# Optimization experiments

Hardware: AMD Instinct MI355X
Metric: run time of the kernel (lower is better)

Reference implementation:

```python
import jax, jax.numpy as jnp
import numpy as np

B, S, D = 2, 2048, 1024
H, HK, HD = 16, 4, 64          # query heads, kv heads, head dim = D//H
WIN = 1024                     # sliding attention window
E, K, DH = 8, 2, 2048          # experts, top_k, expert hidden (== d_head ctor arg)
ATTN_EPS, FFN_EPS = 1e-5, 1e-6
ROPE_THETA = 10000.0


def setup_inputs() -> dict:
    key = jax.random.key(0)
    ks = jax.random.split(key, 9)
    sc = 0.02
    # real rotary frequencies for positions [start_pos, start_pos+S)
    start_pos = 0
    inv_freq = 1.0 / (ROPE_THETA ** (jnp.arange(0, HD, 2, dtype=jnp.float32) / HD))  # [HD//2]
    pos = jnp.arange(start_pos, start_pos + S, dtype=jnp.float32)
    ang = pos[:, None] * inv_freq[None, :]  # [S, HD//2]
    return {
        'x': jax.random.normal(ks[0], (B, S, D), jnp.float32),
        'freqs_cos': jnp.cos(ang),
        'freqs_sin': jnp.sin(ang),
        'attn_norm_w': jnp.ones((D,), jnp.float32),
        'wq': jax.random.normal(ks[1], (D, H * HD), jnp.float32) * sc,
        'wk': jax.random.normal(ks[2], (D, HK * HD), jnp.float32) * sc,
        'wv': jax.random.normal(ks[3], (D, HK * HD), jnp.float32) * sc,
        'wo': jax.random.normal(ks[4], (H * HD, D), jnp.float32) * sc,
        'ffn_norm_w': jnp.ones((D,), jnp.float32),
        'router_w': jax.random.normal(ks[5], (D, E), jnp.float32) * sc,
        'w1': jax.random.normal(ks[6], (E, D, DH), jnp.float32) * sc,
        'w2': jax.random.normal(ks[7], (E, DH, D), jnp.float32) * sc,
        'start_pos': start_pos,
    }


def _rmsnorm(x, w, eps):
    return x * jax.lax.rsqrt(jnp.mean(x * x, axis=-1, keepdims=True) + eps) * w


def _rope(t, cos, sin):
    # t: [B,S,N,HD]; cos/sin: [S,HD//2] -> complex rotation on consecutive pairs
    shp = t.shape
    t = t.reshape(shp[:-1] + (HD // 2, 2))
    t0, t1 = t[..., 0], t[..., 1]
    c = cos[None, :, None, :]
    s = sin[None, :, None, :]
    r = jnp.stack([t0 * c - t1 * s, t0 * s + t1 * c], axis=-1)
    return r.reshape(shp)


def reference(x, freqs_cos, freqs_sin, attn_norm_w, wq, wk, wv, wo,
              ffn_norm_w, router_w, w1, w2, start_pos):
    # ---- attention sublayer (RMSNorm -> GQA sliding-window attn) ----
    hn = _rmsnorm(x, attn_norm_w, ATTN_EPS)
    q = (hn @ wq).reshape(B, S, H, HD)
    k = (hn @ wk).reshape(B, S, HK, HD)
    v = (hn @ wv).reshape(B, S, HK, HD)
    q = _rope(q, freqs_cos, freqs_sin)
    k = _rope(k, freqs_cos, freqs_sin)
    rep = H // HK
    k = jnp.repeat(k, rep, axis=2)  # [B,S,H,HD]
    v = jnp.repeat(v, rep, axis=2)
    scale = 1.0 / np.sqrt(HD).astype(np.float32)
    scores = jnp.einsum('bqhd,bkhd->bhqk', q, k) * scale  # [B,H,S,S]
    qi = jnp.arange(S) + start_pos
    kj = jnp.arange(S) + start_pos
    mask = (kj[None, :] <= qi[:, None]) & (qi[:, None] - kj[None, :] < WIN)
    scores = jnp.where(mask[None, None], scores, jnp.float32(-1e30))
    attn = jax.nn.softmax(scores, axis=-1)
    o = jnp.einsum('bhqk,bkhd->bqhd', attn, v).reshape(B, S, H * HD)
    h = x + o @ wo

    # ---- MoE sublayer (RMSNorm -> router top-k -> expert FFNs) ----
    fn = _rmsnorm(h, ffn_norm_w, FFN_EPS).reshape(-1, D)  # [T,D], T=B*S
    probs = jax.nn.softmax(fn @ router_w, axis=-1)        # [T,E]
    top_vals, top_idx = jax.lax.top_k(probs, K)           # [T,K]
    gates = top_vals / jnp.sum(top_vals, axis=-1, keepdims=True)
    gmat = jnp.sum(jax.nn.one_hot(top_idx, E, dtype=fn.dtype) * gates[..., None], axis=1)  # [T,E]
    moe = jnp.zeros_like(fn)
    for e in range(E):  # fixed small expert count
        moe = moe + gmat[:, e:e + 1] * (jax.nn.silu(fn @ w1[e]) @ w2[e])
    return h + moe.reshape(B, S, D)
```

## Files before the change

kernel.cpp:

```cpp
#include <hip/hip_runtime.h>
#include <hip/hip_bf16.h>

using bf16 = __hip_bfloat16;
typedef __attribute__((ext_vector_type(8))) short bf16x8;
typedef __attribute__((ext_vector_type(4))) short short4v;
typedef __attribute__((ext_vector_type(4))) float f32x4;

#define DEV static __device__ __forceinline__

DEV float b2f(bf16 v) { return __bfloat162float(v); }
DEV bf16  f2b(float f) { return __float2bfloat16(f); }
DEV short bbits(float f) { bf16 h = __float2bfloat16(f); short u; __builtin_memcpy(&u, &h, 2); return u; }
DEV float sb2f(short s) {
  unsigned u = ((unsigned)(unsigned short)s) << 16;
  float f; __builtin_memcpy(&f, &u, 4); return f;
}

#define GL2LDS(g, l)                                                        \
  __builtin_amdgcn_global_load_lds(                                         \
      (const __attribute__((address_space(1))) void*)(g),                   \
      (__attribute__((address_space(3))) void*)(l), 16, 0, 0)

__global__ __launch_bounds__(256) void transpose_convert(
    const float* __restrict__ src, bf16* __restrict__ dst, int K, int N) {
  __shared__ float tile[64][65];
  int n0 = blockIdx.x * 64, k0 = blockIdx.y * 64;
  src += (size_t)blockIdx.z * K * N;
  dst += (size_t)blockIdx.z * K * N;
  int t = threadIdx.x;
  int rr = t >> 4, cc = (t & 15) * 4;
#pragma unroll
  for (int p = 0; p < 4; ++p) {
    int r = rr + p * 16;
    const float4 v = *(const float4*)&src[(size_t)(k0 + r) * N + n0 + cc];
    tile[r][cc] = v.x; tile[r][cc + 1] = v.y; tile[r][cc + 2] = v.z; tile[r][cc + 3] = v.w;
  }
  __syncthreads();
#pragma unroll
  for (int p = 0; p < 4; ++p) {
    int nr = rr + p * 16;
    short4v o;
    o[0] = bbits(tile[cc + 0][nr]);
    o[1] = bbits(tile[cc + 1][nr]);
    o[2] = bbits(tile[cc + 2][nr]);
    o[3] = bbits(tile[cc + 3][nr]);
    *(short4v*)&dst[(size_t)(n0 + nr) * K + k0 + cc] = o;
  }
}

__global__ __launch_bounds__(256) void rmsnorm_kernel(
    const float* __restrict__ x, const float* __restrict__ w,
    bf16* __restrict__ o, float eps) {
  int row = blockIdx.x;
  const float* xr = x + (size_t)row * 1024;
  int t = threadIdx.x;
  float4 v = *(const float4*)&xr[t * 4];
  float ss = v.x * v.x + v.y * v.y + v.z * v.z + v.w * v.w;
#pragma unroll
  for (int d = 32; d; d >>= 1) ss += __shfl_down(ss, d);
  __shared__ float red[4];
  if ((t & 63) == 0) red[t >> 6] = ss;
  __syncthreads();
  float sum = red[0] + red[1] + red[2] + red[3];
  float sc = rsqrtf(sum * (1.f / 1024.f) + eps);
  const float4 wv = *(const float4*)&w[t * 4];
  short4v pk;
  pk[0] = bbits(v.x * sc * wv.x);
  pk[1] = bbits(v.y * sc * wv.y);
  pk[2] = bbits(v.z * sc * wv.z);
  pk[3] = bbits(v.w * sc * wv.w);
  *(short4v*)&o[(size_t)row * 1024 + t * 4] = pk;
}

__global__ __launch_bounds__(256) void rmsnorm_router(
    const float* __restrict__ h, const float* __restrict__ w,
    const float* __restrict__ rw, bf16* __restrict__ fn,
    float* __restrict__ gates, int* __restrict__ eidx) {
  int row = blockIdx.x;
  const float* hr = h + (size_t)row * 1024;
  int t = threadIdx.x;
  float4 v = *(const float4*)&hr[t * 4];
  float ss = v.x * v.x + v.y * v.y + v.z * v.z + v.w * v.w;
#pragma unroll
  for (int d = 32; d; d >>= 1) ss += __shfl_down(ss, d);
  __shared__ float red[4];
  __shared__ float red2[4][8];
  if ((t & 63) == 0) red[t >> 6] = ss;
  __syncthreads();
  float sum = red[0] + red[1] + red[2] + red[3];
  float sc = rsqrtf(sum * (1.f / 1024.f) + 1e-6f);
  const float4 wv = *(const float4*)&w[t * 4];
  float f0 = v.x * sc * wv.x, f1 = v.y * sc * wv.y;
  float f2 = v.z * sc * wv.z, f3 = v.w * sc * wv.w;
  short4v pk;
  pk[0] = bbits(f0); pk[1] = bbits(f1); pk[2] = bbits(f2); pk[3] = bbits(f3);
  *(short4v*)&fn[(size_t)row * 1024 + t * 4] = pk;
  const float* rr = rw + (size_t)t * 4 * 8;
  float lg[8];
#pragma unroll
  for (int e = 0; e < 8; ++e)
    lg[e] = f0 * rr[e] + f1 * rr[8 + e] + f2 * rr[16 + e] + f3 * rr[24 + e];
#pragma unroll
  for (int d = 32; d; d >>= 1)
#pragma unroll
    for (int e = 0; e < 8; ++e) lg[e] += __shfl_down(lg[e], d);
  if ((t & 63) == 0)
#pragma unroll
    for (int e = 0; e < 8; ++e) red2[t >> 6][e] = lg[e];
  __syncthreads();
  if (t == 0) {
    float L[8];
#pragma unroll
    for (int e = 0; e < 8; ++e)
      L[e] = red2[0][e] + red2[1][e] + red2[2][e] + red2[3][e];
    int e0 = 0; float v0 = L[0];
#pragma unroll
    for (int e = 1; e < 8; ++e) if (L[e] > v0) { v0 = L[e]; e0 = e; }
    int e1 = -1; float v1 = -1e30f;
#pragma unroll
    for (int e = 0; e < 8; ++e) if (e != e0 && L[e] > v1) { v1 = L[e]; e1 = e; }
    float r1 = expf(v1 - v0);
    float den = 1.f + r1;
    gates[row * 2] = 1.f / den;
    gates[row * 2 + 1] = r1 / den;
    eidx[row * 2] = e0;
    eidx[row * 2 + 1] = e1;
  }
}

template <int MODE>
__global__ __launch_bounds__(256) void gemm_bt(
    const bf16* __restrict__ A, const bf16* __restrict__ Bt,
    int M, int N, int Kd,
    bf16* __restrict__ outb, bf16* __restrict__ outk, bf16* __restrict__ outv,
    float* __restrict__ outf, const float* __restrict__ resid,
    const float* __restrict__ fcos, const float* __restrict__ fsin,
    const int* __restrict__ counts, const int* __restrict__ offsets,
    const int* __restrict__ tok, const float* __restrict__ gatel) {
  int count = M, off = 0;
  const bf16* Ap = A;
  const bf16* Bp = Bt;
  int mb, nb;
  if (MODE == 2 || MODE == 3) {
    int e = blockIdx.y;
    count = counts[e]; off = offsets[e];
    Bp = Bt + (size_t)e * Kd * N;
    if (MODE == 3) Ap = A + (size_t)off * Kd;
    mb = blockIdx.z * 128; nb = blockIdx.x * 128;
  } else {
    int gx = gridDim.x;
    int flat = blockIdx.y * gx + blockIdx.x;
    int cpx = (gx * gridDim.y) >> 3;
    int swz = (flat & 7) * cpx + (flat >> 3);
    mb = (swz / gx) * 128; nb = (swz % gx) * 128;
  }
  if (mb >= count) return;

  __shared__ __align__(16) bf16 As[2][128 * 32];
  __shared__ __align__(16) bf16 Bs[2][128 * 32];

  int t = threadIdx.x;
  int lane = t & 63, wid = t >> 6;

  const bf16* agl[2];
  const bf16* bgl[2];
#pragma unroll
  for (int iss = 0; iss < 2; ++iss) {
    int p = iss * 256 + wid * 64 + lane;
    int row = p >> 2, cs = p & 3;
    int c = cs ^ (row & 3);
    int m = mb + row;
    const bf16* abase;
    if (MODE == 2) {
      int tokid = (m < count) ? tok[off + m] : 0;
      abase = A + (size_t)tokid * Kd;
    } else {
      int mm = (m < count) ? m : 0;
      abase = Ap + (size_t)mm * Kd;
    }
    agl[iss] = abase + c * 8;
    bgl[iss] = Bp + (size_t)(nb + row) * Kd + c * 8;
  }

  int wr = (wid >> 1) * 64, wc = (wid & 1) * 64;
  int lr = lane & 15, lkc = lane >> 4;

  auto stage = [&](int buf, int kt) {
#pragma unroll
    for (int iss = 0; iss < 2; ++iss) {
      GL2LDS(agl[iss] + kt * 32, &As[buf][(iss * 256 + wid * 64) * 8]);
      GL2LDS(bgl[iss] + kt * 32, &Bs[buf][(iss * 256 + wid * 64) * 8]);
    }
  };

  const f32x4 fzero = {0.f, 0.f, 0.f, 0.f};
  f32x4 acc[4][4];
#pragma unroll
  for (int i = 0; i < 4; ++i)
#pragma unroll
    for (int j = 0; j < 4; ++j) acc[i][j] = fzero;

  int nk = Kd >> 5;
  stage(0, 0);
  __syncthreads();
  for (int kt = 0; kt < nk; ++kt) {
    int cur = kt & 1;
    if (kt + 1 < nk) stage(cur ^ 1, kt + 1);
    bf16x8 af[4], bfr[4];
#pragma unroll
    for (int i = 0; i < 4; ++i) {
      int r = wr + i * 16 + lr;
      af[i] = *(const bf16x8*)&As[cur][r * 32 + ((lkc ^ (r & 3)) * 8)];
    }
#pragma unroll
    for (int j = 0; j < 4; ++j) {
      int r = wc + j * 16 + lr;
      bfr[j] = *(const bf16x8*)&Bs[cur][r * 32 + ((lkc ^ (r & 3)) * 8)];
    }
#pragma unroll
    for (int i = 0; i < 4; ++i)
#pragma unroll
      for (int j = 0; j < 4; ++j)
        acc[i][j] = __builtin_amdgcn_mfma_f32_16x16x32_bf16(af[i], bfr[j], acc[i][j], 0, 0, 0);
    __syncthreads();
  }

  int rq = lane >> 4;
#pragma unroll
  for (int i = 0; i < 4; ++i) {
#pragma unroll
    for (int j = 0; j < 4; ++j) {
      if (MODE == 5) {
        int n = nb + wc + j * 16 + lr;
        if (n >= 1280) {
          int vcol = n - 1280;
          int kh = vcol >> 6, d = vcol & 63;
          int m0 = mb + wr + i * 16 + rq * 4;
          int bb = m0 >> 11, s = m0 & 2047;
          short4v pk;
#pragma unroll
          for (int r = 0; r < 4; ++r) pk[r] = bbits(acc[i][j][r]);
          *(short4v*)&outv[((size_t)((bb * 4 + kh) * 64 + d)) * 2048 + s] = pk;
        } else {
          int ii = (n & 63) >> 1;
          bool odd = n & 1;
#pragma unroll
          for (int r = 0; r < 4; ++r) {
            int m = mb + wr + i * 16 + rq * 4 + r;
            int s = m & 2047;
            float v = acc[i][j][r];
            float vp = __shfl_xor(v, 1);
            float c = fcos[s * 32 + ii], sn = fsin[s * 32 + ii];
            float o = odd ? (vp * sn + v * c) : (v * c - vp * sn);
            if (n < 1024) outb[(size_t)m * 1024 + n] = f2b(o);
            else          outk[(size_t)m * 256 + (n - 1024)] = f2b(o);
          }
        }
      } else {
#pragma unroll
        for (int r = 0; r < 4; ++r) {
          int m = mb + wr + i * 16 + rq * 4 + r;
          int n = nb + wc + j * 16 + lr;
          float v = acc[i][j][r];
          if (MODE == 1) {
            outf[(size_t)m * N + n] = resid[(size_t)m * N + n] + v;
          } else if (MODE == 2) {
            if (m < count) {
              float sg = 1.f / (1.f + expf(-v));
              outb[(size_t)(off + m) * N + n] = f2b(v * sg);
            }
          } else if (MODE == 3) {
            if (m < count) {
              int row = off + m;
              outb[(size_t)row * N + n] = f2b(gatel[row] * v);
            }
          }
        }
      }
    }
  }
}

__global__ __launch_bounds__(256) void attn_kernel(
    const bf16* __restrict__ q, const bf16* __restrict__ kb,
    const bf16* __restrict__ vt, bf16* __restrict__ o) {
  int qb = blockIdx.x, h = blockIdx.y, b = blockIdx.z;
  int kh = h >> 2;
  int t = threadIdx.x;
  int lane = t & 63, wid = t >> 6;
  int lr = lane & 15, lkc = lane >> 4;
  int q0 = qb * 64;
  int qrow = q0 + wid * 16;

  __shared__ __align__(16) bf16 Ks[64 * 64];
  __shared__ __align__(16) bf16 Vs[64 * 64];
  __shared__ __align__(16) bf16 Ps[4][16 * 72];

  bf16x8 aq[2];
#pragma unroll
  for (int kk = 0; kk < 2; ++kk)
    aq[kk] = *(const bf16x8*)&q[(size_t)(b * 2048 + qrow + lr) * 1024 + h * 64 + kk * 32 + lkc * 8];

  const f32x4 fzero = {0.f, 0.f, 0.f, 0.f};
  f32x4 oacc[4];
  float mrun[4], lrun[4];
#pragma unroll
  for (int r = 0; r < 4; ++r) { oacc[r] = fzero; mrun[r] = -1e30f; lrun[r] = 0.f; }

  int klo = q0 - 1023; if (klo < 0) klo = 0;
  int tlo = klo >> 6, thi = q0 >> 6;
  int skey = t >> 3;
  int sch = t & 7;

  for (int kt = tlo; kt <= thi; ++kt) {
    int kbase = kt * 64;
#pragma unroll
    for (int pp = 0; pp < 2; ++pp) {
      int key = skey + pp * 32;
      bf16x8 kv = *(const bf16x8*)&kb[(size_t)(b * 2048 + kbase + key) * 256 + kh * 64 + sch * 8];
      *(bf16x8*)&Ks[key * 64 + ((sch ^ (key & 7)) * 8)] = kv;
      bf16x8 vv = *(const bf16x8*)&vt[((size_t)((b * 4 + kh) * 64 + key)) * 2048 + kbase + sch * 8];
      *(bf16x8*)&Vs[key * 64 + ((sch ^ (key & 7)) * 8)] = vv;
    }
    __syncthreads();

    f32x4 sacc[4];
#pragma unroll
    for (int nt = 0; nt < 4; ++nt) sacc[nt] = fzero;
#pragma unroll
    for (int nt = 0; nt < 4; ++nt)
#pragma unroll
      for (int kk = 0; kk < 2; ++kk) {
        int r = nt * 16 + lr;
        bf16x8 bk = *(const bf16x8*)&Ks[r * 64 + (((kk * 4 + lkc) ^ (r & 7)) * 8)];
        sacc[nt] = __builtin_amdgcn_mfma_f32_16x16x32_bf16(aq[kk], bk, sacc[nt], 0, 0, 0);
      }

    float sval[4][4], mt[4];
    int qg = qrow + lkc * 4;
#pragma unroll
    for (int r = 0; r < 4; ++r) mt[r] = -1e30f;
#pragma unroll
    for (int nt = 0; nt < 4; ++nt) {
      int kkey = kbase + nt * 16 + lr;
#pragma unroll
      for (int r = 0; r < 4; ++r) {
        float s = sacc[nt][r] * 0.125f;
        int qq = qg + r;
        bool valid = (kkey <= qq) && (qq - kkey < 1024);
        s = valid ? s : -1e30f;
        sval[nt][r] = s;
        mt[r] = fmaxf(mt[r], s);
      }
    }
#pragma unroll
    for (int d = 1; d < 16; d <<= 1)
#pragma unroll
      for (int r = 0; r < 4; ++r) mt[r] = fmaxf(mt[r], __shfl_xor(mt[r], d));
    float alpha[4], rs[4];
#pragma unroll
    for (int r = 0; r < 4; ++r) {
      float mn = fmaxf(mrun[r], mt[r]);
      alpha[r] = __expf(mrun[r] - mn);
      mrun[r] = mn;
      rs[r] = 0.f;
    }
#pragma unroll
    for (int nt = 0; nt < 4; ++nt)
#pragma unroll
      for (int r = 0; r < 4; ++r) {
        float pv = __expf(sval[nt][r] - mrun[r]);
        sval[nt][r] = pv;
        rs[r] += pv;
      }
#pragma unroll
    for (int d = 1; d < 16; d <<= 1)
#pragma unroll
      for (int r = 0; r < 4; ++r) rs[r] += __shfl_xor(rs[r], d);
#pragma unroll
    for (int r = 0; r < 4; ++r) lrun[r] = lrun[r] * alpha[r] + rs[r];
#pragma unroll
    for (int dt = 0; dt < 4; ++dt) {
      f32x4 t4 = oacc[dt];
#pragma unroll
      for (int r = 0; r < 4; ++r) t4[r] *= alpha[r];
      oacc[dt] = t4;
    }

    bf16* pw = &Ps[wid][0];
#pragma unroll
    for (int nt = 0; nt < 4; ++nt)
#pragma unroll
      for (int r = 0; r < 4; ++r)
        pw[(lkc * 4 + r) * 72 + nt * 16 + lr] = f2b(sval[nt][r]);
    __syncthreads();

    bf16x8 pa[2];
#pragma unroll
    for (int kk2 = 0; kk2 < 2; ++kk2)
      pa[kk2] = *(const bf16x8*)&pw[lr * 72 + kk2 * 32 + lkc * 8];
#pragma unroll
    for (int dt = 0; dt < 4; ++dt)
#pragma unroll
      for (int kk2 = 0; kk2 < 2; ++kk2) {
        int rrow = dt * 16 + lr;
        bf16x8 bv = *(const bf16x8*)&Vs[rrow * 64 + (((kk2 * 4 + lkc) ^ (rrow & 7)) * 8)];
        oacc[dt] = __builtin_amdgcn_mfma_f32_16x16x32_bf16(pa[kk2], bv, oacc[dt], 0, 0, 0);
      }
    __syncthreads();
  }

#pragma unroll
  for (int dt = 0; dt < 4; ++dt)
#pragma unroll
    for (int r = 0; r < 4; ++r) {
      int qq = qrow + lkc * 4 + r;
      int dd = dt * 16 + lr;
      o[(size_t)(b * 2048 + qq) * 1024 + h * 64 + dd] = f2b(oacc[dt][r] / lrun[r]);
    }
}

__global__ __launch_bounds__(1024) void moe_setup(
    const int* __restrict__ eidx, const float* __restrict__ gates,
    int* __restrict__ counts, int* __restrict__ offsets,
    int* __restrict__ tok, float* __restrict__ gatel, int* __restrict__ inv) {
  __shared__ int hist[8];
  __shared__ int cur[8];
  int t = threadIdx.x;
  if (t < 8) hist[t] = 0;
  __syncthreads();
  int e[8];
#pragma unroll
  for (int c = 0; c < 8; ++c) {
    e[c] = eidx[c * 1024 + t];
    atomicAdd(&hist[e[c]], 1);
  }
  __syncthreads();
  if (t == 0) {
    int o = 0;
#pragma unroll
    for (int i = 0; i < 8; ++i) {
      offsets[i] = o; cur[i] = o;
      int cnt = hist[i]; counts[i] = cnt; o += cnt;
    }
  }
  __syncthreads();
#pragma unroll
  for (int c = 0; c < 8; ++c) {
    int i = c * 1024 + t;
    int pos = atomicAdd(&cur[e[c]], 1);
    tok[pos] = i >> 1;
    gatel[pos] = gates[i];
    inv[i] = pos;
  }
}

__global__ __launch_bounds__(256) void final_add(
    const float* __restrict__ h, const bf16* __restrict__ y2,
    const int* __restrict__ inv, float* __restrict__ out) {
  int tokid = blockIdx.x;
  int t = threadIdx.x;
  int i0 = inv[tokid * 2], i1 = inv[tokid * 2 + 1];
  size_t base = (size_t)tokid * 1024 + t * 4;
  float4 a = *(const float4*)&h[base];
  short4v p0 = *(const short4v*)&y2[(size_t)i0 * 1024 + t * 4];
  short4v p1 = *(const short4v*)&y2[(size_t)i1 * 1024 + t * 4];
  float4 o;
  o.x = a.x + sb2f(p0[0]) + sb2f(p1[0]);
  o.y = a.y + sb2f(p0[1]) + sb2f(p1[1]);
  o.z = a.z + sb2f(p0[2]) + sb2f(p1[2]);
  o.w = a.w + sb2f(p0[3]) + sb2f(p1[3]);
  *(float4*)&out[base] = o;
}

extern "C" void kernel_launch(void* const* d_in, const int* in_sizes, int n_in,
                              void* d_out, int out_size, void* d_ws, size_t ws_size,
                              hipStream_t stream) {
  const float* x    = (const float*)d_in[0];
  const float* fcos = (const float*)d_in[1];
  const float* fsin = (const float*)d_in[2];
  const float* attw = (const float*)d_in[3];
  const float* wq   = (const float*)d_in[4];
  const float* wk   = (const float*)d_in[5];
  const float* wv   = (const float*)d_in[6];
  const float* wo   = (const float*)d_in[7];
  const float* ffnw = (const float*)d_in[8];
  const float* rw   = (const float*)d_in[9];
  const float* w1   = (const float*)d_in[10];
  const float* w2   = (const float*)d_in[11];
  float* out = (float*)d_out;

  const int M = 4096;
  char* p = (char*)d_ws;
  auto alloc = [&](size_t b) { char* r = p; p += (b + 255) & ~(size_t)255; return r; };

  bf16* hn     = (bf16*)alloc((size_t)M * 1024 * 2);
  bf16* qb     = (bf16*)alloc((size_t)M * 1024 * 2);
  bf16* kbuf   = (bf16*)alloc((size_t)M * 256 * 2);
  bf16* vt     = (bf16*)alloc((size_t)M * 256 * 2);
  bf16* ob     = (bf16*)alloc((size_t)M * 1024 * 2);
  float* hbuf  = (float*)alloc((size_t)M * 1024 * 4);
  bf16* fn     = (bf16*)alloc((size_t)M * 1024 * 2);
  bf16* wqkvt  = (bf16*)alloc((size_t)1536 * 1024 * 2);
  bf16* wot    = (bf16*)alloc((size_t)1024 * 1024 * 2);
  bf16* w1t    = (bf16*)alloc((size_t)8 * 2048 * 1024 * 2);
  bf16* w2t    = (bf16*)alloc((size_t)8 * 1024 * 2048 * 2);
  bf16* act    = (bf16*)alloc((size_t)8192 * 2048 * 2);
  bf16* y2     = (bf16*)alloc((size_t)8192 * 1024 * 2);
  float* gates = (float*)alloc((size_t)M * 2 * 4);
  int* eidx    = (int*)alloc((size_t)M * 2 * 4);
  int* counts  = (int*)alloc(8 * 4);
  int* offsets = (int*)alloc(8 * 4);
  int* tok     = (int*)alloc(8192 * 4);
  int* inv     = (int*)alloc(8192 * 4);
  float* gatel = (float*)alloc(8192 * 4);

  transpose_convert<<<dim3(16, 16, 1), 256, 0, stream>>>(wq, wqkvt, 1024, 1024);
  transpose_convert<<<dim3(4, 16, 1), 256, 0, stream>>>(wk, wqkvt + (size_t)1024 * 1024, 1024, 256);
  transpose_convert<<<dim3(4, 16, 1), 256, 0, stream>>>(wv, wqkvt + (size_t)1280 * 1024, 1024, 256);
  transpose_convert<<<dim3(16, 16, 1), 256, 0, stream>>>(wo, wot, 1024, 1024);
  transpose_convert<<<dim3(32, 16, 8), 256, 0, stream>>>(w1, w1t, 1024, 2048);
  transpose_convert<<<dim3(16, 32, 8), 256, 0, stream>>>(w2, w2t, 2048, 1024);

  rmsnorm_kernel<<<M, 256, 0, stream>>>(x, attw, hn, 1e-5f);

  gemm_bt<5><<<dim3(12, 32, 1), 256, 0, stream>>>(hn, wqkvt, M, 1536, 1024,
      qb, kbuf, vt, nullptr, nullptr, fcos, fsin, nullptr, nullptr, nullptr, nullptr);

  attn_kernel<<<dim3(32, 16, 2), 256, 0, stream>>>(qb, kbuf, vt, ob);

  gemm_bt<1><<<dim3(8, 32, 1), 256, 0, stream>>>(ob, wot, M, 1024, 1024,
      nullptr, nullptr, nullptr, hbuf, x, nullptr, nullptr, nullptr, nullptr, nullptr, nullptr);

  rmsnorm_router<<<M, 256, 0, stream>>>(hbuf, ffnw, rw, fn, gates, eidx);
  moe_setup<<<1, 1024, 0, stream>>>(eidx, gates, counts, offsets, tok, gatel, inv);

  gemm_bt<2><<<dim3(16, 8, 64), 256, 0, stream>>>(fn, w1t, M, 2048, 1024,
      act, nullptr, nullptr, nullptr, nullptr, nullptr, nullptr, counts, offsets, tok, nullptr);
  gemm_bt<3><<<dim3(8, 8, 64), 256, 0, stream>>>(act, w2t, M, 1024, 2048,
      y2, nullptr, nullptr, nullptr, nullptr, nullptr, nullptr, counts, offsets, tok, gatel);

  final_add<<<M, 256, 0, stream>>>(hbuf, y2, inv, out);
}
```

Measured before the change: 354.1 us.

## Add dedicated 256x128-tile MoE up-projection GEMM with 512 threads and 3-stage B pipeline

Replaces the generic gemm_bt<2> expert up-projection with a specialized kernel that uses 256-row M tiles, 8 waves per block, and a triple-buffered B / double-buffered A LDS pipeline with explicit vmcnt waits and raised MFMA priority. The larger M tile halves the number of times each expert weight tile is streamed and reduces the block count, and the deeper pipeline is meant to hide global-to-LDS latency. It trades higher LDS and register use (launch_bounds 512,1) and more wasted rows for experts whose token count is not a multiple of 256. Padding rows now clamp to the last valid token instead of token 0.

```diff
diff --git a/kernel.cpp b/kernel.cpp
--- a/kernel.cpp
+++ b/kernel.cpp
@@ -125,6 +125,120 @@
     gates[row * 2 + 1] = r1 / den;
     eidx[row * 2] = e0;
     eidx[row * 2 + 1] = e1;
+  }
+}
+
+__global__ __launch_bounds__(512, 1) void gemm_moe1(
+    const bf16* __restrict__ A, const bf16* __restrict__ Bt,
+    bf16* __restrict__ outb,
+    const int* __restrict__ counts, const int* __restrict__ offsets,
+    const int* __restrict__ tok) {
+  constexpr int Kd = 1024;
+  constexpr int NN = 2048;
+  constexpr int nk = Kd / 32;
+  int e = blockIdx.y;
+  int count = counts[e], off = offsets[e];
+  int mb = blockIdx.z * 256, nb = blockIdx.x * 128;
+  if (mb >= count) return;
+  const bf16* Bp = Bt + (size_t)e * Kd * NN;
+
+  __shared__ __align__(16) bf16 As[2][256 * 32];
+  __shared__ __align__(16) bf16 Bs[3][128 * 32];
+
+  int t = threadIdx.x;
+  int lane = t & 63, wid = t >> 6;
+  int wm = wid >> 1, wn = wid & 1;
+  int lr = lane & 15, rq = lane >> 4;
+
+  const bf16* aptr[2];
+  int adst[2];
+#pragma unroll
+  for (int l = 0; l < 2; ++l) {
+    int c = l * 512 + t;
+    int row = c >> 2, slot = c & 3;
+    int kc = slot ^ (row & 3);
+    int m = mb + row;
+    int mm = (m < count) ? m : (count - 1);
+    aptr[l] = A + (size_t)tok[off + mm] * Kd + kc * 8;
+    adst[l] = c * 8;
+  }
+  int brow = t >> 2, bslot = t & 3;
+  int bkc = bslot ^ (brow & 3);
+  const bf16* bptr = Bp + (size_t)(nb + brow) * Kd + bkc * 8;
+  int bdst = t * 8;
+
+  const f32x4 fzero = {0.f, 0.f, 0.f, 0.f};
+  f32x4 acc[4][4];
+#pragma unroll
+  for (int i = 0; i < 4; ++i)
+#pragma unroll
+    for (int j = 0; j < 4; ++j) acc[i][j] = fzero;
+
+  {
+    GL2LDS(aptr[0], &As[0][adst[0]]);
+    GL2LDS(aptr[1], &As[0][adst[1]]);
+    GL2LDS(bptr, &Bs[0][bdst]);
+    GL2LDS(aptr[0] + 32, &As[1][adst[0]]);
+    GL2LDS(aptr[1] + 32, &As[1][adst[1]]);
+    GL2LDS(bptr + 32, &Bs[1][bdst]);
+  }
+
+  int bs = 0;
+  for (int kt = 0; kt < nk; ++kt) {
+    int as = kt & 1;
+    if (kt == nk - 1) {
+      asm volatile("s_waitcnt vmcnt(0)" ::: "memory");
+    } else {
+      asm volatile("s_waitcnt vmcnt(3)" ::: "memory");
+    }
+    __builtin_amdgcn_s_barrier();
+    __builtin_amdgcn_sched_barrier(0);
+    int bs2 = bs + 2; if (bs2 >= 3) bs2 -= 3;
+    if (kt + 2 < nk) {
+      GL2LDS(bptr + (kt + 2) * 32, &Bs[bs2][bdst]);
+    }
+    bf16x8 af[4], bfr[4];
+#pragma unroll
+    for (int i = 0; i < 4; ++i) {
+      int r = wm * 64 + i * 16 + lr;
+      af[i] = *(const bf16x8*)&As[as][r * 32 + ((rq ^ (r & 3)) * 8)];
+    }
+#pragma unroll
+    for (int j = 0; j < 4; ++j) {
+      int r = wn * 64 + j * 16 + lr;
+      bfr[j] = *(const bf16x8*)&Bs[bs][r * 32 + ((rq ^ (r & 3)) * 8)];
+    }
+    __builtin_amdgcn_s_setprio(1);
+#pragma unroll
+    for (int i = 0; i < 4; ++i)
+#pragma unroll
+      for (int j = 0; j < 4; ++j)
+        acc[i][j] = __builtin_amdgcn_mfma_f32_16x16x32_bf16(af[i], bfr[j], acc[i][j], 0, 0, 0);
+    __builtin_amdgcn_s_setprio(0);
+    __builtin_amdgcn_sched_barrier(0);
+    __builtin_amdgcn_s_barrier();
+    if (kt + 2 < nk) {
+      GL2LDS(aptr[0] + (kt + 2) * 32, &As[as][adst[0]]);
+      GL2LDS(aptr[1] + (kt + 2) * 32, &As[as][adst[1]]);
+    }
+    ++bs; if (bs == 3) bs = 0;
+  }
+
+#pragma unroll
+  for (int i = 0; i < 4; ++i) {
+#pragma unroll
+    for (int j = 0; j < 4; ++j) {
+#pragma unroll
+      for (int r = 0; r < 4; ++r) {
+        int m = mb + wm * 64 + i * 16 + rq * 4 + r;
+        if (m < count) {
+          int n = nb + wn * 64 + j * 16 + lr;
+          float v = acc[i][j][r];
+          float sg = 1.f / (1.f + expf(-v));
+          outb[(size_t)(off + m) * 2048 + n] = f2b(v * sg);
+        }
+      }
+    }
   }
 }
 
@@ -141,11 +255,11 @@
   const bf16* Ap = A;
   const bf16* Bp = Bt;
   int mb, nb;
-  if (MODE == 2 || MODE == 3) {
+  if (MODE == 3) {
     int e = blockIdx.y;
     count = counts[e]; off = offsets[e];
     Bp = Bt + (size_t)e * Kd * N;
-    if (MODE == 3) Ap = A + (size_t)off * Kd;
+    Ap = A + (size_t)off * Kd;
     mb = blockIdx.z * 128; nb = blockIdx.x * 128;
   } else {
     int gx = gridDim.x;
@@ -170,14 +284,9 @@
     int row = p >> 2, cs = p & 3;
     int c = cs ^ (row & 3);
     int m = mb + row;
-    const bf16* abase;
-    if (MODE == 2) {
-      int tokid = (m < count) ? tok[off + m] : 0;
-      abase = A + (size_t)tokid * Kd;
-    } else {
-      int mm = (m < count) ? m : 0;
-      abase = Ap + (size_t)mm * Kd;
-    }
+    int mm = (m < count) ? m : (count > 0 ? count - 1 : 0);
+    const bf16* abase = Ap + (size_t)((MODE == 3) ? mm : m) * Kd;
+    if (MODE != 3) abase = Ap + (size_t)m * Kd;
     agl[iss] = abase + c * 8;
     bgl[iss] = Bp + (size_t)(nb + row) * Kd + c * 8;
   }
@@ -264,11 +373,6 @@
           float v = acc[i][j][r];
           if (MODE == 1) {
             outf[(size_t)m * N + n] = resid[(size_t)m * N + n] + v;
-          } else if (MODE == 2) {
-            if (m < count) {
-              float sg = 1.f / (1.f + expf(-v));
-              outb[(size_t)(off + m) * N + n] = f2b(v * sg);
-            }
           } else if (MODE == 3) {
             if (m < count) {
               int row = off + m;
@@ -535,8 +639,7 @@
   rmsnorm_router<<<M, 256, 0, stream>>>(hbuf, ffnw, rw, fn, gates, eidx);
   moe_setup<<<1, 1024, 0, stream>>>(eidx, gates, counts, offsets, tok, gatel, inv);
 
-  gemm_bt<2><<<dim3(16, 8, 64), 256, 0, stream>>>(fn, w1t, M, 2048, 1024,
-      act, nullptr, nullptr, nullptr, nullptr, nullptr, nullptr, counts, offsets, tok, nullptr);
+  gemm_moe1<<<dim3(16, 8, 32), 512, 0, stream>>>(fn, w1t, act, counts, offsets, tok);
   gemm_bt<3><<<dim3(8, 8, 64), 256, 0, stream>>>(act, w2t, M, 1024, 2048,
       y2, nullptr, nullptr, nullptr, nullptr, nullptr, nullptr, counts, offsets, tok, gatel);
 
```

Result: slower. 393.8 us (+11.2%).

## Schedule MoE expert GEMMs over a compact grouped tile list

Applied to the files above, without the earlier changes.

Replaces the MoE grouped GEMMs, which launched a fixed grid of experts times 64 row-tiles and had most blocks exit early, with a dedicated kernel. It builds a prefix sum of per-expert tile counts and has a grid-stride loop over only the tiles that exist. Dimensions are now compile-time constants, and the dense GEMM loses its MoE branches. This removes empty-block launch overhead and balances work across CUs, at the cost of a per-block prefix scan and fixed grid sizes.

```diff
diff --git a/kernel.cpp b/kernel.cpp
--- a/kernel.cpp
+++ b/kernel.cpp
@@ -134,27 +134,12 @@
     int M, int N, int Kd,
     bf16* __restrict__ outb, bf16* __restrict__ outk, bf16* __restrict__ outv,
     float* __restrict__ outf, const float* __restrict__ resid,
-    const float* __restrict__ fcos, const float* __restrict__ fsin,
-    const int* __restrict__ counts, const int* __restrict__ offsets,
-    const int* __restrict__ tok, const float* __restrict__ gatel) {
-  int count = M, off = 0;
-  const bf16* Ap = A;
-  const bf16* Bp = Bt;
-  int mb, nb;
-  if (MODE == 2 || MODE == 3) {
-    int e = blockIdx.y;
-    count = counts[e]; off = offsets[e];
-    Bp = Bt + (size_t)e * Kd * N;
-    if (MODE == 3) Ap = A + (size_t)off * Kd;
-    mb = blockIdx.z * 128; nb = blockIdx.x * 128;
-  } else {
-    int gx = gridDim.x;
-    int flat = blockIdx.y * gx + blockIdx.x;
-    int cpx = (gx * gridDim.y) >> 3;
-    int swz = (flat & 7) * cpx + (flat >> 3);
-    mb = (swz / gx) * 128; nb = (swz % gx) * 128;
-  }
-  if (mb >= count) return;
+    const float* __restrict__ fcos, const float* __restrict__ fsin) {
+  int gx = gridDim.x;
+  int flat = blockIdx.y * gx + blockIdx.x;
+  int cpx = (gx * gridDim.y) >> 3;
+  int swz = (flat & 7) * cpx + (flat >> 3);
+  int mb = (swz / gx) * 128, nb = (swz % gx) * 128;
 
   __shared__ __align__(16) bf16 As[2][128 * 32];
   __shared__ __align__(16) bf16 Bs[2][128 * 32];
@@ -169,17 +154,8 @@
     int p = iss * 256 + wid * 64 + lane;
     int row = p >> 2, cs = p & 3;
     int c = cs ^ (row & 3);
-    int m = mb + row;
-    const bf16* abase;
-    if (MODE == 2) {
-      int tokid = (m < count) ? tok[off + m] : 0;
-      abase = A + (size_t)tokid * Kd;
-    } else {
-      int mm = (m < count) ? m : 0;
-      abase = Ap + (size_t)mm * Kd;
-    }
-    agl[iss] = abase + c * 8;
-    bgl[iss] = Bp + (size_t)(nb + row) * Kd + c * 8;
+    agl[iss] = A + (size_t)(mb + row) * Kd + c * 8;
+    bgl[iss] = Bt + (size_t)(nb + row) * Kd + c * 8;
   }
 
   int wr = (wid >> 1) * 64, wc = (wid & 1) * 64;
@@ -261,18 +237,118 @@
         for (int r = 0; r < 4; ++r) {
           int m = mb + wr + i * 16 + rq * 4 + r;
           int n = nb + wc + j * 16 + lr;
-          float v = acc[i][j][r];
-          if (MODE == 1) {
-            outf[(size_t)m * N + n] = resid[(size_t)m * N + n] + v;
-          } else if (MODE == 2) {
-            if (m < count) {
+          outf[(size_t)m * N + n] = resid[(size_t)m * N + n] + acc[i][j][r];
+        }
+      }
+    }
+  }
+}
+
+template <int MODE>
+__global__ __launch_bounds__(256) void gemm_moe(
+    const bf16* __restrict__ A, const bf16* __restrict__ Bt,
+    bf16* __restrict__ outb,
+    const int* __restrict__ counts, const int* __restrict__ offsets,
+    const int* __restrict__ tok, const float* __restrict__ gatel) {
+  constexpr int NDIM = (MODE == 2) ? 2048 : 1024;
+  constexpr int KD   = (MODE == 2) ? 1024 : 2048;
+  constexpr int nk   = KD >> 5;
+  int nb = blockIdx.x * 128;
+
+  int pre[9];
+  pre[0] = 0;
+#pragma unroll
+  for (int e = 0; e < 8; ++e) pre[e + 1] = pre[e] + ((counts[e] + 127) >> 7);
+  int total = pre[8];
+
+  __shared__ __align__(16) bf16 As[2][128 * 32];
+  __shared__ __align__(16) bf16 Bs[2][128 * 32];
+
+  int t = threadIdx.x;
+  int lane = t & 63, wid = t >> 6;
+  int wr = (wid >> 1) * 64, wc = (wid & 1) * 64;
+  int lr = lane & 15, lkc = lane >> 4;
+  int rq = lane >> 4;
+
+  for (int g = blockIdx.y; g < total; g += gridDim.y) {
+    int e = 0;
+#pragma unroll
+    for (int k = 0; k < 7; ++k) e += (g >= pre[e + 1]) ? 1 : 0;
+    int count = counts[e], off = offsets[e];
+    int mb = (g - pre[e]) * 128;
+    const bf16* Bp = Bt + (size_t)e * (size_t)KD * NDIM;
+
+    const bf16* agl[2];
+    const bf16* bgl[2];
+#pragma unroll
+    for (int iss = 0; iss < 2; ++iss) {
+      int p = iss * 256 + wid * 64 + lane;
+      int row = p >> 2, cs = p & 3;
+      int c = cs ^ (row & 3);
+      int m = mb + row;
+      int mm = (m < count) ? m : (count - 1);
+      const bf16* abase;
+      if (MODE == 2) abase = A + (size_t)tok[off + mm] * KD;
+      else           abase = A + (size_t)(off + mm) * KD;
+      agl[iss] = abase + c * 8;
+      bgl[iss] = Bp + (size_t)(nb + row) * KD + c * 8;
+    }
+
+    auto stage = [&](int buf, int kt) {
+#pragma unroll
+      for (int iss = 0; iss < 2; ++iss) {
+        GL2LDS(agl[iss] + kt * 32, &As[buf][(iss * 256 + wid * 64) * 8]);
+        GL2LDS(bgl[iss] + kt * 32, &Bs[buf][(iss * 256 + wid * 64) * 8]);
+      }
+    };
+
+    const f32x4 fzero = {0.f, 0.f, 0.f, 0.f};
+    f32x4 acc[4][4];
+#pragma unroll
+    for (int i = 0; i < 4; ++i)
+#pragma unroll
+      for (int j = 0; j < 4; ++j) acc[i][j] = fzero;
+
+    stage(0, 0);
+    __syncthreads();
+    for (int kt = 0; kt < nk; ++kt) {
+      int cur = kt & 1;
+      if (kt + 1 < nk) stage(cur ^ 1, kt + 1);
+      bf16x8 af[4], bfr[4];
+#pragma unroll
+      for (int i = 0; i < 4; ++i) {
+        int r = wr + i * 16 + lr;
+        af[i] = *(const bf16x8*)&As[cur][r * 32 + ((lkc ^ (r & 3)) * 8)];
+      }
+#pragma unroll
+      for (int j = 0; j < 4; ++j) {
+        int r = wc + j * 16 + lr;
+        bfr[j] = *(const bf16x8*)&Bs[cur][r * 32 + ((lkc ^ (r & 3)) * 8)];
+      }
+#pragma unroll
+      for (int i = 0; i < 4; ++i)
+#pragma unroll
+        for (int j = 0; j < 4; ++j)
+          acc[i][j] = __builtin_amdgcn_mfma_f32_16x16x32_bf16(af[i], bfr[j], acc[i][j], 0, 0, 0);
+      __syncthreads();
+    }
+
+#pragma unroll
+    for (int i = 0; i < 4; ++i) {
+#pragma unroll
+      for (int j = 0; j < 4; ++j) {
+#pragma unroll
+        for (int r = 0; r < 4; ++r) {
+          int m = mb + wr + i * 16 + rq * 4 + r;
+          if (m < count) {
+            int n = nb + wc + j * 16 + lr;
+            float v = acc[i][j][r];
+            if (MODE == 2) {
               float sg = 1.f / (1.f + expf(-v));
-              outb[(size_t)(off + m) * N + n] = f2b(v * sg);
-            }
-          } else if (MODE == 3) {
-            if (m < count) {
+              outb[(size_t)(off + m) * NDIM + n] = f2b(v * sg);
+            } else {
               int row = off + m;
-              outb[(size_t)row * N + n] = f2b(gatel[row] * v);
+              outb[(size_t)row * NDIM + n] = f2b(gatel[row] * v);
             }
           }
         }
@@ -525,20 +601,18 @@
   rmsnorm_kernel<<<M, 256, 0, stream>>>(x, attw, hn, 1e-5f);
 
   gemm_bt<5><<<dim3(12, 32, 1), 256, 0, stream>>>(hn, wqkvt, M, 1536, 1024,
-      qb, kbuf, vt, nullptr, nullptr, fcos, fsin, nullptr, nullptr, nullptr, nullptr);
+      qb, kbuf, vt, nullptr, nullptr, fcos, fsin);
 
   attn_kernel<<<dim3(32, 16, 2), 256, 0, stream>>>(qb, kbuf, vt, ob);
 
   gemm_bt<1><<<dim3(8, 32, 1), 256, 0, stream>>>(ob, wot, M, 1024, 1024,
-      nullptr, nullptr, nullptr, hbuf, x, nullptr, nullptr, nullptr, nullptr, nullptr, nullptr);
+      nullptr, nullptr, nullptr, hbuf, x, nullptr, nullptr);
 
   rmsnorm_router<<<M, 256, 0, stream>>>(hbuf, ffnw, rw, fn, gates, eidx);
   moe_setup<<<1, 1024, 0, stream>>>(eidx, gates, counts, offsets, tok, gatel, inv);
 
-  gemm_bt<2><<<dim3(16, 8, 64), 256, 0, stream>>>(fn, w1t, M, 2048, 1024,
-      act, nullptr, nullptr, nullptr, nullptr, nullptr, nullptr, counts, offsets, tok, nullptr);
-  gemm_bt<3><<<dim3(8, 8, 64), 256, 0, stream>>>(act, w2t, M, 1024, 2048,
-      y2, nullptr, nullptr, nullptr, nullptr, nullptr, nullptr, counts, offsets, tok, gatel);
+  gemm_moe<2><<<dim3(16, 64, 1), 256, 0, stream>>>(fn, w1t, act, counts, offsets, tok, nullptr);
+  gemm_moe<3><<<dim3(8, 128, 1), 256, 0, stream>>>(act, w2t, y2, counts, offsets, tok, gatel);
 
   final_add<<<M, 256, 0, stream>>>(hbuf, y2, inv, out);
 }
```

After: 421.7 us. 1.19x slower.
